# Performance work log

Hardware: AMD Instinct MI355X
Metric: run time of the kernel (lower is better)

## Reference

```python
import jax, jax.numpy as jnp
import numpy as np

NH, NW = 5, 5          # attn_neighborhood_size (odd -> symmetric 'same' padding)
HEADS, HEAD_DIM = 8, 64
DIM = 512              # == heads*head_dim, but project_out=True since heads>1
B, HMAP, WMAP = 4, 64, 64
N = HMAP * WMAP


def local_expand(t, height, width):
    """Equivalent of impulse-filter conv2d neighbor gather.

    t: [b, heads, n, d] -> [b, heads, n, NH*NW, d]
    neighbor f=(i,j) of pixel (p,q) is t[p+i-NH//2, q+j-NW//2], zero-padded.
    """
    b, h, n, d = t.shape
    y = t.reshape(b, h, height, width, d)
    ph, pw = NH // 2, NW // 2
    yp = jnp.pad(y, ((0, 0), (0, 0), (ph, ph), (pw, pw), (0, 0)))
    # fixed small loop over the 25 window offsets (row-major = filter order)
    slabs = [yp[:, :, i:i + height, j:j + width, :]
             for i in range(NH) for j in range(NW)]
    out = jnp.stack(slabs, axis=4)  # [b, h, H, W, F, d]
    return out.reshape(b, h, n, NH * NW, d)


def setup_inputs() -> dict:
    key = jax.random.key(0)
    k1, k2, k3, k4 = jax.random.split(key, 4)
    inner = HEADS * HEAD_DIM
    x = jax.random.normal(k1, (B, N, DIM), dtype=jnp.float32)
    # torch Linear weights are [out_features, in_features]
    w_qkv = jax.random.normal(k2, (3 * inner, DIM), dtype=jnp.float32) * (DIM ** -0.5)
    w_out = jax.random.normal(k3, (DIM, inner), dtype=jnp.float32) * (inner ** -0.5)
    b_out = jax.random.normal(k4, (DIM,), dtype=jnp.float32) * 0.01
    return {"x": x, "w_qkv": w_qkv, "w_out": w_out, "b_out": b_out,
            "h": HMAP, "w": WMAP}


def reference(x, w_qkv, w_out, b_out, h, w):
    b, n, _ = x.shape
    scale = HEAD_DIM ** -0.5
    qkv = x @ w_qkv.T                                   # [b, n, 3*inner]
    q, k, v = jnp.split(qkv, 3, axis=-1)
    def to_heads(t):
        return t.reshape(b, n, HEADS, HEAD_DIM).transpose(0, 2, 1, 3)  # b h n d
    q, k, v = to_heads(q), to_heads(k), to_heads(v)
    k_loc = local_expand(k, h, w)                       # [b, h, n, F, d]
    v_loc = local_expand(v, h, w)
    dots = jnp.einsum('bhnd,bhnfd->bhnf', q, k_loc) * scale
    attn = jax.nn.softmax(dots, axis=-1)
    out = jnp.einsum('bhnf,bhnfd->bhnd', attn, v_loc)   # [b, h, n, d]
    out = out.transpose(0, 2, 1, 3).reshape(b, n, HEADS * HEAD_DIM)
    return out @ w_out.T + b_out                        # dropout=0 (eval)
```

## Files before the change

kernel.cpp:

```cpp
#include <hip/hip_runtime.h>
#include <cstddef>
#include <cstdint>


namespace {

typedef short s16x8 __attribute__((ext_vector_type(8)));
typedef unsigned short u16x8 __attribute__((ext_vector_type(8)));
typedef float f32x4 __attribute__((ext_vector_type(4)));

constexpr int kHeads = 8;
constexpr int kN = 4096;
constexpr float kScale = 0.125f;

__device__ inline float blo(unsigned u) {
  return __uint_as_float(u << 16);
}
__device__ inline float bhi(unsigned u) {
  return __uint_as_float(u & 0xffff0000u);
}
__device__ inline unsigned short f2b(float x) {
  unsigned u = __float_as_uint(x);
  return (unsigned short)((u + 0x7fffu + ((u >> 16) & 1u)) >> 16);
}

__device__ __forceinline__ float dot2bf(float d, unsigned a, unsigned b) {
  asm("v_dot2_f32_bf16 %0, %1, %2, %0" : "+v"(d) : "v"(a), "v"(b));
  return d;
}

__device__ __forceinline__ void g2l16(const unsigned short* g,
                                      unsigned short* l) {
  __builtin_amdgcn_global_load_lds(
      (const __attribute__((address_space(1))) void*)g,
      (__attribute__((address_space(3))) void*)l, 16, 0, 0);
}

__global__ __launch_bounds__(256) void cvt_all(
    const float* __restrict__ wq, const float* __restrict__ wo,
    const float* __restrict__ x, unsigned short* __restrict__ wqb,
    unsigned short* __restrict__ wob, unsigned short* __restrict__ xb,
    unsigned short* __restrict__ zp) {
  const int i = blockIdx.x * 256 + threadIdx.x;
  if (i < 16) ((unsigned long long*)zp)[i] = 0ull;
  const float* src;
  unsigned short* dst;
  int off;
  if (i < 98304) {
    src = wq; dst = wqb; off = i;
  } else if (i < 131072) {
    src = wo; dst = wob; off = i - 98304;
  } else {
    src = x; dst = xb; off = i - 131072;
  }
  const float4 a = ((const float4*)src)[off * 2];
  const float4 b = ((const float4*)src)[off * 2 + 1];
  u16x8 o;
  o[0] = f2b(a.x); o[1] = f2b(a.y); o[2] = f2b(a.z); o[3] = f2b(a.w);
  o[4] = f2b(b.x); o[5] = f2b(b.y); o[6] = f2b(b.z); o[7] = f2b(b.w);
  *(u16x8*)(dst + (size_t)off * 8) = o;
}

__device__ __forceinline__ void stage64(const unsigned short* __restrict__ A,
                                        const unsigned short* __restrict__ W,
                                        int m0, int n0, int k0, int wv,
                                        int rsub, int slog,
                                        unsigned short* As,
                                        unsigned short* Bs) {
#pragma unroll
  for (int it = 0; it < 4; ++it) {
    const int g = wv * 4 + it;
    const int row = g * 8 + rsub;
    g2l16(A + (size_t)(m0 + row) * 512 + k0 + slog * 8, As + g * 512);
    g2l16(W + (size_t)(n0 + row) * 512 + k0 + slog * 8, Bs + g * 512);
  }
}

__device__ __forceinline__ void mfma_512(const unsigned short* __restrict__ A,
                                         const unsigned short* __restrict__ W,
                                         int m0, int n0, int tid,
                                         unsigned short* As, unsigned short* Bs,
                                         f32x4 (&acc)[4][4]) {
  const int lane = tid & 63;
  const int wv = tid >> 6;
  const int wm = wv & 1, wn = wv >> 1;
  const int rsub = lane >> 3;
  const int slog = (lane & 7) ^ rsub;
#pragma unroll
  for (int i = 0; i < 4; ++i)
#pragma unroll
    for (int j = 0; j < 4; ++j) acc[i][j] = f32x4{0.f, 0.f, 0.f, 0.f};

  stage64(A, W, m0, n0, 0, wv, rsub, slog, As, Bs);
  __syncthreads();
  int buf = 0;
  for (int k = 0; k < 8; ++k) {
    if (k < 7)
      stage64(A, W, m0, n0, (k + 1) * 64, wv, rsub, slog,
              As + (buf ^ 1) * 8192, Bs + (buf ^ 1) * 8192);
    const unsigned short* as = As + buf * 8192;
    const unsigned short* bs = Bs + buf * 8192;
#pragma unroll
    for (int kh = 0; kh < 2; ++kh) {
      s16x8 af[4], bf[4];
      const int q = kh * 4 + (lane >> 4);
#pragma unroll
      for (int i = 0; i < 4; ++i) {
        const int Ra = wm * 64 + i * 16 + (lane & 15);
        af[i] = *(const s16x8*)&as[Ra * 64 + ((q ^ (Ra & 7)) * 8)];
        const int Rb = wn * 64 + i * 16 + (lane & 15);
        bf[i] = *(const s16x8*)&bs[Rb * 64 + ((q ^ (Rb & 7)) * 8)];
      }
#pragma unroll
      for (int i = 0; i < 4; ++i)
#pragma unroll
        for (int j = 0; j < 4; ++j)
          acc[i][j] = __builtin_amdgcn_mfma_f32_16x16x32_bf16(
              af[i], bf[j], acc[i][j], 0, 0, 0);
    }
    __syncthreads();
    buf ^= 1;
  }
}

__global__ __launch_bounds__(256, 3) void gemm_qkv(
    const unsigned short* __restrict__ A, const unsigned short* __restrict__ W,
    unsigned short* __restrict__ Qb, unsigned short* __restrict__ Kb,
    unsigned short* __restrict__ Vb) {
  __shared__ unsigned short As[16384], Bs[16384];
  const int tid = threadIdx.x;
  const int id = blockIdx.x;
  const int xcd = id & 7;
  const int j = id >> 3;
  const int by = xcd * 16 + j / 12;
  const int bx = j % 12;
  f32x4 acc[4][4];
  mfma_512(A, W, by * 128, bx * 128, tid, As, Bs, acc);

  const int lane = tid & 63;
  const int wv = tid >> 6;
  const int wm = wv & 1, wn = wv >> 1;
  const int cn = bx * 128 + wn * 64;
  unsigned short* dst = (cn < 512) ? Qb : (cn < 1024 ? Kb : Vb);
  const int head = (cn >> 6) & 7;
  const int colb = lane & 15;
#pragma unroll
  for (int mi = 0; mi < 4; ++mi) {
#pragma unroll
    for (int r = 0; r < 4; ++r) {
      const int m = by * 128 + wm * 64 + mi * 16 + (lane >> 4) * 4 + r;
      const int b = m >> 12;
      const int p = m & 4095;
      unsigned short* o =
          dst + ((size_t)(b * kHeads + head) * kN + p) * 64 + colb;
#pragma unroll
      for (int ni = 0; ni < 4; ++ni) o[ni * 16] = f2b(acc[mi][ni][r]);
    }
  }
}

__global__ __launch_bounds__(256, 3) void gemm_out(
    const unsigned short* __restrict__ A, const unsigned short* __restrict__ W,
    const float* __restrict__ bias, float* __restrict__ out) {
  __shared__ unsigned short As[16384], Bs[16384];
  const int tid = threadIdx.x;
  const int id = blockIdx.x;
  const int xcd = id & 7;
  const int j = id >> 3;
  const int by = xcd * 16 + (j >> 2);
  const int bx = j & 3;
  f32x4 acc[4][4];
  mfma_512(A, W, by * 128, bx * 128, tid, As, Bs, acc);

  const int lane = tid & 63;
  const int wv = tid >> 6;
  const int wm = wv & 1, wn = wv >> 1;
  float bvr[4];
#pragma unroll
  for (int ni = 0; ni < 4; ++ni)
    bvr[ni] = bias[bx * 128 + wn * 64 + ni * 16 + (lane & 15)];
#pragma unroll
  for (int mi = 0; mi < 4; ++mi) {
#pragma unroll
    for (int r = 0; r < 4; ++r) {
      const int m = by * 128 + wm * 64 + mi * 16 + (lane >> 4) * 4 + r;
      float* o = out + (size_t)m * 512 + bx * 128 + wn * 64 + (lane & 15);
#pragma unroll
      for (int ni = 0; ni < 4; ++ni) o[ni * 16] = acc[mi][ni][r] + bvr[ni];
    }
  }
}

__global__ __launch_bounds__(256) void attn_q4(
    const unsigned short* __restrict__ Q, const unsigned short* __restrict__ K,
    const unsigned short* __restrict__ V, const unsigned short* __restrict__ Zp,
    unsigned short* __restrict__ AO) {
  __shared__ unsigned short H[2 * 144 * 64];
  const int tid = threadIdx.x;
  const int id = blockIdx.x;
  const int wv = tid >> 6;
  const int xcd = id & 7;
  const int k8 = id >> 3;
  const int bh = xcd * 4 + (k8 >> 6);
  const int tile = k8 & 63;
  const int ty0 = (tile >> 3) * 8, tx0 = (tile & 7) * 8;
  const size_t base = (size_t)bh * kN;
  const int pix = tid >> 2;
  const int sub = tid & 3;
  const int pyl = pix >> 3, pxl = pix & 7;
  const int p = (ty0 + pyl) * 64 + tx0 + pxl;

  const unsigned short* qp = Q + (base + p) * 64 + sub * 16;
  const uint4 qa = *(const uint4*)qp;
  const uint4 qb = *(const uint4*)(qp + 8);

#pragma unroll
  for (int it = 0; it < 5; ++it) {
    const int i = it * 256 + tid;
    if (i < 1152) {
      const int r = i >> 3;
      const int cg = (tid & 7) ^ (r & 7);
      const int gy = ty0 - 2 + r / 12;
      const int gx = tx0 - 2 + r % 12;
      const unsigned short* src =
          ((unsigned)gy < 64u && (unsigned)gx < 64u)
              ? K + (base + (size_t)(gy * 64 + gx)) * 64 + cg * 8
              : Zp + cg * 8;
      g2l16(src, &H[(it * 32 + wv * 8) * 64]);
    }
  }
#pragma unroll
  for (int it = 0; it < 5; ++it) {
    const int i = it * 256 + tid;
    if (i < 1152) {
      const int r = i >> 3;
      const int cg = (tid & 7) ^ (r & 7);
      const int gy = ty0 - 2 + r / 12;
      const int gx = tx0 - 2 + r % 12;
      const unsigned short* src =
          ((unsigned)gy < 64u && (unsigned)gx < 64u)
              ? V + (base + (size_t)(gy * 64 + gx)) * 64 + cg * 8
              : Zp + cg * 8;
      g2l16(src, &H[9216 + (it * 32 + wv * 8) * 64]);
    }
  }

  asm volatile("s_waitcnt vmcnt(4)" ::: "memory");
  __builtin_amdgcn_s_barrier();
  __builtin_amdgcn_sched_barrier(0);

  float dots[25];
#pragma unroll
  for (int fy = 0; fy < 5; ++fy) {
#pragma unroll
    for (int fx = 0; fx < 5; ++fx) {
      const int row = (pyl + fy) * 12 + pxl + fx;
      const int swz = (row & 7) << 3;
      const unsigned short* hr = &H[row * 64];
      const uint4 ka = *(const uint4*)(hr + ((sub * 16) ^ swz));
      const uint4 kb = *(const uint4*)(hr + ((sub * 16 + 8) ^ swz));
      float d = 0.f;
      d = dot2bf(d, qa.x, ka.x);
      d = dot2bf(d, qa.y, ka.y);
      d = dot2bf(d, qa.z, ka.z);
      d = dot2bf(d, qa.w, ka.w);
      d = dot2bf(d, qb.x, kb.x);
      d = dot2bf(d, qb.y, kb.y);
      d = dot2bf(d, qb.z, kb.z);
      d = dot2bf(d, qb.w, kb.w);
      dots[fy * 5 + fx] = d;
    }
  }

#pragma unroll
  for (int f = 0; f < 25; ++f) {
    dots[f] += __shfl_xor(dots[f], 1, 64);
    dots[f] += __shfl_xor(dots[f], 2, 64);
  }

  float mx = -1e30f;
#pragma unroll
  for (int f = 0; f < 25; ++f) {
    dots[f] *= kScale;
    mx = fmaxf(mx, dots[f]);
  }
  float sum = 0.f;
#pragma unroll
  for (int f = 0; f < 25; ++f) {
    dots[f] = __expf(dots[f] - mx);
    sum += dots[f];
  }
  const float inv = 1.f / sum;
#pragma unroll
  for (int f = 0; f < 25; ++f) dots[f] *= inv;

  asm volatile("s_waitcnt vmcnt(0)" ::: "memory");
  __builtin_amdgcn_s_barrier();
  __builtin_amdgcn_sched_barrier(0);

  const int b = bh >> 3, h = bh & 7;
  unsigned short* op = AO + ((size_t)(b * kN + p)) * 512 + h * 64 + sub * 16;
#pragma unroll 1
  for (int hh = 0; hh < 2; ++hh) {
    float o[8];
#pragma unroll
    for (int j = 0; j < 8; ++j) o[j] = 0.f;
#pragma unroll
    for (int fy = 0; fy < 5; ++fy) {
#pragma unroll
      for (int fx = 0; fx < 5; ++fx) {
        const int row = (pyl + fy) * 12 + pxl + fx;
        const int swz = (row & 7) << 3;
        const uint4 va =
            *(const uint4*)&H[9216 + row * 64 + ((sub * 16 + hh * 8) ^ swz)];
        const float wf = dots[fy * 5 + fx];
        o[0] = fmaf(wf, blo(va.x), o[0]);
        o[1] = fmaf(wf, bhi(va.x), o[1]);
        o[2] = fmaf(wf, blo(va.y), o[2]);
        o[3] = fmaf(wf, bhi(va.y), o[3]);
        o[4] = fmaf(wf, blo(va.z), o[4]);
        o[5] = fmaf(wf, bhi(va.z), o[5]);
        o[6] = fmaf(wf, blo(va.w), o[6]);
        o[7] = fmaf(wf, bhi(va.w), o[7]);
      }
    }
    u16x8 pk;
#pragma unroll
    for (int j = 0; j < 8; ++j) pk[j] = f2b(o[j]);
    *(u16x8*)(op + hh * 8) = pk;
  }
}

}

extern "C" void kernel_launch(void* const* d_in, const int* in_sizes, int n_in,
                              void* d_out, int out_size, void* d_ws,
                              size_t ws_size, hipStream_t stream) {
  (void)in_sizes; (void)n_in; (void)out_size; (void)ws_size;
  const float* x = (const float*)d_in[0];
  const float* w_qkv = (const float*)d_in[1];
  const float* w_out = (const float*)d_in[2];
  const float* b_out = (const float*)d_in[3];
  float* out = (float*)d_out;

  unsigned short* ws0 = (unsigned short*)d_ws;
  unsigned short* wqkvb = ws0;
  unsigned short* woutb = ws0 + 786432;
  unsigned short* xb = ws0 + 1048576;
  unsigned short* Qb = ws0 + 9437184;
  unsigned short* Kb = ws0 + 17825792;
  unsigned short* Vb = ws0 + 26214400;
  unsigned short* AO = ws0 + 34603008;
  unsigned short* Zp = ws0 + 42991616;

  cvt_all<<<4608, 256, 0, stream>>>(w_qkv, w_out, x, wqkvb, woutb, xb, Zp);
  gemm_qkv<<<1536, 256, 0, stream>>>(xb, wqkvb, Qb, Kb, Vb);
  attn_q4<<<2048, 256, 0, stream>>>(Qb, Kb, Vb, Zp, AO);
  gemm_out<<<512, 256, 0, stream>>>(AO, woutb, b_out, out);
}
```

Before: 191.5 us.

## Use vmcnt-based waits in double-buffered QKV GEMM, single-buffer output GEMM

The QKV projection GEMM keeps double buffering but replaces the __syncthreads barriers with explicit s_waitcnt vmcnt(8) plus s_barrier. This lets the next tile's global-to-LDS loads stay in flight while the current tile is computed. The output projection GEMM switches to a single-buffered loop with half the shared memory, aiming for higher occupancy at the cost of exposing load latency. Hand-written waitcnt counts depend on how many memory ops stage64 issues, so they could cause races if the compiler emits a different number.

```diff
diff --git a/kernel.cpp b/kernel.cpp
--- a/kernel.cpp
+++ b/kernel.cpp
@@ -76,6 +76,30 @@
   }
 }
 
+__device__ __forceinline__ void compute64(const unsigned short* __restrict__ as,
+                                          const unsigned short* __restrict__ bs,
+                                          int lane, int wm, int wn,
+                                          f32x4 (&acc)[4][4]) {
+#pragma unroll
+  for (int kh = 0; kh < 2; ++kh) {
+    s16x8 af[4], bf[4];
+    const int q = kh * 4 + (lane >> 4);
+#pragma unroll
+    for (int i = 0; i < 4; ++i) {
+      const int Ra = wm * 64 + i * 16 + (lane & 15);
+      af[i] = *(const s16x8*)&as[Ra * 64 + ((q ^ (Ra & 7)) * 8)];
+      const int Rb = wn * 64 + i * 16 + (lane & 15);
+      bf[i] = *(const s16x8*)&bs[Rb * 64 + ((q ^ (Rb & 7)) * 8)];
+    }
+#pragma unroll
+    for (int i = 0; i < 4; ++i)
+#pragma unroll
+      for (int j = 0; j < 4; ++j)
+        acc[i][j] = __builtin_amdgcn_mfma_f32_16x16x32_bf16(
+            af[i], bf[j], acc[i][j], 0, 0, 0);
+  }
+}
+
 __device__ __forceinline__ void mfma_512(const unsigned short* __restrict__ A,
                                          const unsigned short* __restrict__ W,
                                          int m0, int n0, int tid,
@@ -91,34 +115,43 @@
 #pragma unroll
     for (int j = 0; j < 4; ++j) acc[i][j] = f32x4{0.f, 0.f, 0.f, 0.f};
 
+  for (int k0 = 0; k0 < 512; k0 += 64) {
+    stage64(A, W, m0, n0, k0, wv, rsub, slog, As, Bs);
+    __syncthreads();
+    compute64(As, Bs, lane, wm, wn, acc);
+    __syncthreads();
+  }
+}
+
+__device__ __forceinline__ void mfma_512_db(
+    const unsigned short* __restrict__ A, const unsigned short* __restrict__ W,
+    int m0, int n0, int tid, unsigned short* As, unsigned short* Bs,
+    f32x4 (&acc)[4][4]) {
+  const int lane = tid & 63;
+  const int wv = tid >> 6;
+  const int wm = wv & 1, wn = wv >> 1;
+  const int rsub = lane >> 3;
+  const int slog = (lane & 7) ^ rsub;
+#pragma unroll
+  for (int i = 0; i < 4; ++i)
+#pragma unroll
+    for (int j = 0; j < 4; ++j) acc[i][j] = f32x4{0.f, 0.f, 0.f, 0.f};
+
   stage64(A, W, m0, n0, 0, wv, rsub, slog, As, Bs);
-  __syncthreads();
   int buf = 0;
+#pragma unroll 1
   for (int k = 0; k < 8; ++k) {
     if (k < 7)
       stage64(A, W, m0, n0, (k + 1) * 64, wv, rsub, slog,
               As + (buf ^ 1) * 8192, Bs + (buf ^ 1) * 8192);
-    const unsigned short* as = As + buf * 8192;
-    const unsigned short* bs = Bs + buf * 8192;
-#pragma unroll
-    for (int kh = 0; kh < 2; ++kh) {
-      s16x8 af[4], bf[4];
-      const int q = kh * 4 + (lane >> 4);
-#pragma unroll
-      for (int i = 0; i < 4; ++i) {
-        const int Ra = wm * 64 + i * 16 + (lane & 15);
-        af[i] = *(const s16x8*)&as[Ra * 64 + ((q ^ (Ra & 7)) * 8)];
-        const int Rb = wn * 64 + i * 16 + (lane & 15);
-        bf[i] = *(const s16x8*)&bs[Rb * 64 + ((q ^ (Rb & 7)) * 8)];
-      }
-#pragma unroll
-      for (int i = 0; i < 4; ++i)
-#pragma unroll
-        for (int j = 0; j < 4; ++j)
-          acc[i][j] = __builtin_amdgcn_mfma_f32_16x16x32_bf16(
-              af[i], bf[j], acc[i][j], 0, 0, 0);
-    }
-    __syncthreads();
+    if (k < 7)
+      asm volatile("s_waitcnt vmcnt(8)" ::: "memory");
+    else
+      asm volatile("s_waitcnt vmcnt(0)" ::: "memory");
+    asm volatile("s_barrier" ::: "memory");
+    __builtin_amdgcn_sched_barrier(0);
+    compute64(As + buf * 8192, Bs + buf * 8192, lane, wm, wn, acc);
+    asm volatile("s_barrier" ::: "memory");
     buf ^= 1;
   }
 }
@@ -135,7 +168,7 @@
   const int by = xcd * 16 + j / 12;
   const int bx = j % 12;
   f32x4 acc[4][4];
-  mfma_512(A, W, by * 128, bx * 128, tid, As, Bs, acc);
+  mfma_512_db(A, W, by * 128, bx * 128, tid, As, Bs, acc);
 
   const int lane = tid & 63;
   const int wv = tid >> 6;
@@ -162,7 +195,7 @@
 __global__ __launch_bounds__(256, 3) void gemm_out(
     const unsigned short* __restrict__ A, const unsigned short* __restrict__ W,
     const float* __restrict__ bias, float* __restrict__ out) {
-  __shared__ unsigned short As[16384], Bs[16384];
+  __shared__ unsigned short As[8192], Bs[8192];
   const int tid = threadIdx.x;
   const int id = blockIdx.x;
   const int xcd = id & 7;
```

Measured after the change: 173.5 us. 1.1x faster.
